# Performance work log

Hardware: AMD Instinct MI355X
Metric: run time of the kernel (lower is better)

Reference implementation:

```python
import jax, jax.numpy as jnp
import numpy as np

N = 524288
L = 16          # num_levels
F = 2           # per_level_dim
T = 1 << 19     # hashmap size per level
BASE, MAXR = 32, 2048
SCALE = np.exp(np.log(MAXR / BASE) / (L - 1))
RES = [int(np.floor(BASE * SCALE ** lv)) + 1 for lv in range(L)]
ACTIVE = 4 * F  # init_active_level * per_level_dim (progressive mask)
D_HID = 64
N_FREQS = 6

_P1 = jnp.uint32(2654435761)
_P2 = jnp.uint32(805459861)
_OFF = jnp.array([[(c >> d) & 1 for d in range(3)] for c in range(8)], dtype=jnp.uint32)  # [8,3]


def setup_inputs() -> dict:
    key = jax.random.key(0)
    ks = jax.random.split(key, 8)
    x = (jax.random.uniform(ks[0], (N, 3)) * 2.0 - 1.0) * 0.999  # inside [-bound, bound]
    v = jax.random.normal(ks[1], (N, 3))
    v = v / jnp.linalg.norm(v, axis=-1, keepdims=True)
    o = jax.random.normal(ks[2], (N, 3))  # unused by forward (kept for signature fidelity)
    table = jax.random.uniform(ks[3], (L, T, F), minval=-1e-4, maxval=1e-4)
    d_in = 3 + 3 * 2 * N_FREQS + L * F  # xyz + fourier + hashgrid = 71
    def lin(k, fi, fo):
        return jax.random.normal(k, (fi, fo)) * np.sqrt(2.0 / fi).astype(np.float32)
    dw1 = lin(ks[4], d_in, D_HID); db1 = jnp.zeros((D_HID,), jnp.float32)
    dw2 = lin(ks[5], D_HID, 1 + D_HID); db2 = jnp.zeros((1 + D_HID,), jnp.float32)
    rw1 = lin(ks[6], D_HID + 9, D_HID); rb1 = jnp.zeros((D_HID,), jnp.float32)
    rw2 = lin(ks[7], D_HID, 3); rb2 = jnp.zeros((3,), jnp.float32)
    return dict(x=x, v=v, o=o, table=table, dw1=dw1, db1=db1, dw2=dw2, db2=db2,
                rw1=rw1, rb1=rb1, rw2=rw2, rb2=rb2)


def hashgrid(x01, table):
    """Multi-res hash encoding with Smoothstep interpolation. x01 in [0,1]^3."""
    feats = []
    for lv in range(L):
        pos = x01 * RES[lv]
        p0 = jnp.floor(pos)
        t = pos - p0
        w = t * t * (3.0 - 2.0 * t)                       # smoothstep weights [N,3]
        corner = p0.astype(jnp.uint32)[:, None, :] + _OFF[None]  # [N,8,3]
        h = (corner[..., 0] ^ (corner[..., 1] * _P1) ^ (corner[..., 2] * _P2)) & jnp.uint32(T - 1)
        cw = jnp.prod(jnp.where(_OFF[None] == 1, w[:, None, :], 1.0 - w[:, None, :]), axis=-1)  # [N,8]
        feats.append(jnp.sum(table[lv][h.astype(jnp.int32)] * cw[..., None], axis=1))  # [N,F]
    return jnp.concatenate(feats, axis=-1)  # [N, L*F]


def fourier(x):
    freqs = 2.0 ** jnp.arange(N_FREQS, dtype=x.dtype)  # log-sampled 2^0..2^5
    ang = x[..., None] * freqs                         # [N,3,6]
    return jnp.concatenate([jnp.sin(ang), jnp.cos(ang)], axis=-1).reshape(x.shape[0], -1)


def sh3(d):
    """Spherical harmonics, degree 3 (levels=3) -> 9 features."""
    xx, yy, zz = d[..., 0], d[..., 1], d[..., 2]
    return jnp.stack([
        0.28209479177387814 * jnp.ones_like(xx),
        -0.4886025119029199 * yy, 0.4886025119029199 * zz, -0.4886025119029199 * xx,
        1.0925484305920792 * xx * yy, -1.0925484305920792 * yy * zz,
        0.9461746957575601 * zz * zz - 0.31539156525252005,
        -1.0925484305920792 * xx * zz,
        0.5462742152960396 * (xx * xx - yy * yy)], axis=-1)


def reference(x, v, o, table, dw1, db1, dw2, db2, rw1, rb1, rw2, rb2):
    x01 = (x + 1.0) * 0.5  # bound = 1.0
    grid = hashgrid(x01, table)
    mask = (jnp.arange(L * F) < ACTIVE).astype(grid.dtype)  # progressive level mask
    x_enc = jnp.concatenate([x, fourier(x), grid * mask], axis=-1)  # [N,71]
    h = jax.nn.relu(x_enc @ dw1 + db1)
    dout = h @ dw2 + db2                 # [N, 1 + d_hidden]
    sigma = jnp.exp(dout[..., :1])       # trunc_exp forward == exp
    feat = jax.nn.relu(dout[..., 1:])
    rgb_in = jnp.concatenate([feat, sh3(v)], axis=-1)  # [N, 73]
    hr = jax.nn.relu(rgb_in @ rw1 + rb1)
    rgb = jax.nn.sigmoid(hr @ rw2 + rb2)
    return sigma, rgb
```

## Files before the change

### kernel.cpp

```cpp
#include <hip/hip_runtime.h>

#define NPTS   524288
#define TBLM   ((1u << 19) - 1u)
#define THR    512
#define CHUNK  128
#define CHUNKS 4
#define GRID   (NPTS / (CHUNK * CHUNKS))

typedef _Float16 half8  __attribute__((ext_vector_type(8)));
typedef _Float16 half4v __attribute__((ext_vector_type(4)));
typedef float    f32x4  __attribute__((ext_vector_type(4)));


__global__ __launch_bounds__(256)
void prep(const float* __restrict__ dw1, const float* __restrict__ db1,
          const float* __restrict__ dw2, const float* __restrict__ db2,
          const float* __restrict__ rw1, const float* __restrict__ rb1,
          const float* __restrict__ rw2, const float* __restrict__ rb2,
          void* __restrict__ ws)
{
    const int t = blockIdx.x * 256 + threadIdx.x;
    if (t < 16384) {
        float w = 0.0f;
        if (t < 4096) {
            const int u = t, mkc = u >> 9, m = mkc >> 1, kc = mkc & 1;
            const int lane = (u >> 3) & 63, j = u & 7;
            const int row = 16 * m + (lane & 15);
            const int kp  = kc * 32 + (lane >> 4) * 8 + j;
            if (kp < 39)      w = dw1[kp * 64 + row];
            else if (kp == 39) w = 0.0f;
            else if (kp < 48) w = dw1[(kp - 1) * 64 + row];
        } else if (t < 9216) {
            const int u = t - 4096, mkc = u >> 9, m = mkc >> 1, kc = mkc & 1;
            const int lane = (u >> 3) & 63, j = u & 7;
            const int row = 16 * m + (lane & 15);
            const int k   = kc * 32 + (lane >> 4) * 8 + j;
            if (row < 65) w = dw2[k * 65 + row];
        } else if (t < 15360) {
            const int u = t - 9216, mkc = u >> 9, m = mkc / 3, kc = mkc - 3 * m;
            const int lane = (u >> 3) & 63, j = u & 7;
            const int row = 16 * m + (lane & 15);
            const int kp  = kc * 32 + (lane >> 4) * 8 + j;
            if (kp >= 1 && kp <= 73) w = rw1[(kp - 1) * 64 + row];
        } else {
            const int u = t - 15360, kc = u >> 9;
            const int lane = (u >> 3) & 63, j = u & 7;
            const int row = lane & 15;
            const int k   = kc * 32 + (lane >> 4) * 8 + j;
            if (row < 3) w = rw2[k * 3 + row];
        }
        ((_Float16*)ws)[t] = (_Float16)w;
    } else if (t < 16384 + 224) {
        const int u = t - 16384;
        float b = 0.0f;
        if (u < 64)        b = db1[u];
        else if (u < 144)  { const int r = u - 64;  if (r < 65) b = db2[r]; }
        else if (u < 208)  b = rb1[u - 144];
        else               { const int r = u - 208; if (r < 3)  b = rb2[r]; }
        ((float*)((char*)ws + 32768))[u] = b;
    }
}

__device__ __forceinline__ float sstep(float t) { return t * t * (3.0f - 2.0f * t); }

__global__ __launch_bounds__(THR, 4)
void nerf_fwd(const float* __restrict__ x,
              const float* __restrict__ v,
              const float* __restrict__ table,
              const float* __restrict__ ws,
              float* __restrict__ out)
{
    __shared__ __align__(16) unsigned char smem[78720];
    _Float16* wt    = (_Float16*)smem;
    float*    sbias = (float*)(smem + 32768);
    _Float16* aB    = (_Float16*)(smem + 33664);
    _Float16* bB    = (_Float16*)(smem + 60288);

    const int tid  = threadIdx.x;
    const int lane = tid & 63;
    const int wv   = tid >> 6;
    const int lr   = lane & 15;
    const int lg   = lane >> 4;

    {
        const uint4* src = (const uint4*)ws;
        uint4* dst = (uint4*)smem;
        #pragma unroll
        for (int i = 0; i < 5; ++i) {
            const int idx = tid + i * THR;
            if (idx < 2104) dst[idx] = src[idx];
        }
    }
    __syncthreads();

    const int gi0 = blockIdx.x * (CHUNK * CHUNKS);

    for (int c = 0; c < CHUNKS; ++c) {
        const int cbase = gi0 + c * CHUNK;

        {
            const int p    = (wv << 4) + (lane >> 2);
            const int gi   = cbase + p;
            const int role = lane & 3;
            _Float16* row = aB + p * 104;
            if (role == 3) {
                const float v0 = v[3 * gi + 0], v1 = v[3 * gi + 1], v2 = v[3 * gi + 2];
                float sh[9];
                sh[0] = 0.28209479177387814f;
                sh[1] = -0.4886025119029199f * v1;
                sh[2] =  0.4886025119029199f * v2;
                sh[3] = -0.4886025119029199f * v0;
                sh[4] =  1.0925484305920792f * v0 * v1;
                sh[5] = -1.0925484305920792f * v1 * v2;
                sh[6] =  0.9461746957575601f * v2 * v2 - 0.31539156525252005f;
                sh[7] = -1.0925484305920792f * v0 * v2;
                sh[8] =  0.5462742152960396f * (v0 * v0 - v1 * v1);
                half8 s0, s1, z;
                s0[0] = (_Float16)0.f;
                #pragma unroll
                for (int i = 0; i < 7; ++i) s0[i + 1] = (_Float16)sh[i];
                s1[0] = (_Float16)sh[7]; s1[1] = (_Float16)sh[8];
                #pragma unroll
                for (int i = 2; i < 8; ++i) s1[i] = (_Float16)0.f;
                #pragma unroll
                for (int i = 0; i < 8; ++i) z[i] = (_Float16)0.f;
                *(half8*)(row + 48) = z;
                *(half8*)(row + 56) = z;
                *(half8*)(row + 64) = s0;
                *(half8*)(row + 72) = s1;
                *(half8*)(row + 80) = z;
                *(half8*)(row + 88) = z;
            } else {
                const float x0 = x[3 * gi + 0], x1 = x[3 * gi + 1], x2 = x[3 * gi + 2];
                if (role == 0) {
                    float e[40];
                    e[0] = x0; e[1] = x1; e[2] = x2;
                    const float a[3] = {x0, x1, x2};
                    #pragma unroll
                    for (int d = 0; d < 3; ++d)
                        #pragma unroll
                        for (int f = 0; f < 6; ++f) {
                            const float ang = a[d] * (float)(1 << f);
                            e[3 + d * 12 + f]     = __sinf(ang);
                            e[3 + d * 12 + 6 + f] = __cosf(ang);
                        }
                    e[39] = 0.0f;
                    #pragma unroll
                    for (int chk = 0; chk < 5; ++chk) {
                        half8 h;
                        #pragma unroll
                        for (int i = 0; i < 8; ++i) h[i] = (_Float16)e[chk * 8 + i];
                        *(half8*)(row + chk * 8) = h;
                    }
                } else {
                    const float u0 = (x0 + 1.0f) * 0.5f, u1 = (x1 + 1.0f) * 0.5f, u2 = (x2 + 1.0f) * 0.5f;
                    const float rfA = (role == 1) ? 33.0f : 56.0f;
                    const float rfB = (role == 1) ? 43.0f : 74.0f;
                    const unsigned lvA = (role == 1) ? 0u : 2u;
                    float g[4];
                    #pragma unroll
                    for (int s = 0; s < 2; ++s) {
                        const float rf = s ? rfB : rfA;
                        const unsigned lv = lvA + (unsigned)s;
                        const float px = u0 * rf, py = u1 * rf, pz = u2 * rf;
                        const float fx = floorf(px), fy = floorf(py), fz = floorf(pz);
                        const float wx = sstep(px - fx), wy = sstep(py - fy), wz = sstep(pz - fz);
                        const unsigned cx = (unsigned)fx, cy = (unsigned)fy, cz = (unsigned)fz;
                        float g0 = 0.f, g1 = 0.f;
                        #pragma unroll
                        for (int cc = 0; cc < 8; ++cc) {
                            const unsigned hx = cx + (cc & 1);
                            const unsigned hy = cy + ((cc >> 1) & 1);
                            const unsigned hz = cz + ((cc >> 2) & 1);
                            const unsigned hh = (hx ^ (hy * 2654435761u) ^ (hz * 805459861u)) & TBLM;
                            const float2 tv = *reinterpret_cast<const float2*>(
                                table + (lv * (TBLM + 1u) + hh) * 2u);
                            const float cw = ((cc & 1) ? wx : 1.0f - wx) *
                                             ((cc & 2) ? wy : 1.0f - wy) *
                                             ((cc & 4) ? wz : 1.0f - wz);
                            g0 = fmaf(cw, tv.x, g0);
                            g1 = fmaf(cw, tv.y, g1);
                        }
                        g[2 * s]     = g0;
                        g[2 * s + 1] = g1;
                    }
                    half4v h4;
                    #pragma unroll
                    for (int i = 0; i < 4; ++i) h4[i] = (_Float16)g[i];
                    *(half4v*)(row + 40 + (role - 1) * 4) = h4;
                }
            }
        }

        const int pt = (wv << 4) + lr;

        {
            const half8 B0 = *(const half8*)(aB + pt * 104 + 0 * 32 + lg * 8);
            const half8 B1 = *(const half8*)(aB + pt * 104 + 1 * 32 + lg * 8);
            #pragma unroll
            for (int m = 0; m < 4; ++m) {
                const half8 A0 = *(const half8*)(wt + (m * 2 + 0) * 512 + lane * 8);
                const half8 A1 = *(const half8*)(wt + (m * 2 + 1) * 512 + lane * 8);
                f32x4 cr = *(const f32x4*)(sbias + 0 + m * 16 + 4 * lg);
                cr = __builtin_amdgcn_mfma_f32_16x16x32_f16(A0, B0, cr, 0, 0, 0);
                cr = __builtin_amdgcn_mfma_f32_16x16x32_f16(A1, B1, cr, 0, 0, 0);
                half4v o4;
                #pragma unroll
                for (int r = 0; r < 4; ++r) o4[r] = (_Float16)fmaxf(cr[r], 0.f);
                *(half4v*)(bB + pt * 72 + 16 * m + 4 * lg) = o4;
            }
        }

        {
            const half8 B0 = *(const half8*)(bB + pt * 72 + 0 * 32 + lg * 8);
            const half8 B1 = *(const half8*)(bB + pt * 72 + 1 * 32 + lg * 8);
            #pragma unroll
            for (int m = 0; m < 4; ++m) {
                const half8 A0 = *(const half8*)(wt + 4096 + (m * 2 + 0) * 512 + lane * 8);
                const half8 A1 = *(const half8*)(wt + 4096 + (m * 2 + 1) * 512 + lane * 8);
                f32x4 cr = *(const f32x4*)(sbias + 64 + m * 16 + 4 * lg);
                cr = __builtin_amdgcn_mfma_f32_16x16x32_f16(A0, B0, cr, 0, 0, 0);
                cr = __builtin_amdgcn_mfma_f32_16x16x32_f16(A1, B1, cr, 0, 0, 0);
                half4v o4;
                #pragma unroll
                for (int r = 0; r < 4; ++r) o4[r] = (_Float16)fmaxf(cr[r], 0.f);
                *(half4v*)(aB + pt * 104 + 16 * m + 4 * lg) = o4;
                if (m == 0 && lg == 0)
                    out[cbase + pt] = __expf(cr[0]);
            }
            {
                const half8 A0 = *(const half8*)(wt + 4096 + (4 * 2 + 0) * 512 + lane * 8);
                const half8 A1 = *(const half8*)(wt + 4096 + (4 * 2 + 1) * 512 + lane * 8);
                f32x4 cr = *(const f32x4*)(sbias + 64 + 4 * 16 + 4 * lg);
                cr = __builtin_amdgcn_mfma_f32_16x16x32_f16(A0, B0, cr, 0, 0, 0);
                cr = __builtin_amdgcn_mfma_f32_16x16x32_f16(A1, B1, cr, 0, 0, 0);
                if (lg == 0) aB[pt * 104 + 64] = (_Float16)fmaxf(cr[0], 0.f);
            }
        }

        {
            const half8 B0 = *(const half8*)(aB + pt * 104 + 0 * 32 + lg * 8);
            const half8 B1 = *(const half8*)(aB + pt * 104 + 1 * 32 + lg * 8);
            const half8 B2 = *(const half8*)(aB + pt * 104 + 2 * 32 + lg * 8);
            #pragma unroll
            for (int m = 0; m < 4; ++m) {
                const half8 A0 = *(const half8*)(wt + 9216 + (m * 3 + 0) * 512 + lane * 8);
                const half8 A1 = *(const half8*)(wt + 9216 + (m * 3 + 1) * 512 + lane * 8);
                const half8 A2 = *(const half8*)(wt + 9216 + (m * 3 + 2) * 512 + lane * 8);
                f32x4 cr = *(const f32x4*)(sbias + 144 + m * 16 + 4 * lg);
                cr = __builtin_amdgcn_mfma_f32_16x16x32_f16(A0, B0, cr, 0, 0, 0);
                cr = __builtin_amdgcn_mfma_f32_16x16x32_f16(A1, B1, cr, 0, 0, 0);
                cr = __builtin_amdgcn_mfma_f32_16x16x32_f16(A2, B2, cr, 0, 0, 0);
                half4v o4;
                #pragma unroll
                for (int r = 0; r < 4; ++r) o4[r] = (_Float16)fmaxf(cr[r], 0.f);
                *(half4v*)(bB + pt * 72 + 16 * m + 4 * lg) = o4;
            }
        }

        {
            const half8 A0 = *(const half8*)(wt + 15360 + 0 * 512 + lane * 8);
            const half8 A1 = *(const half8*)(wt + 15360 + 1 * 512 + lane * 8);
            const half8 B0 = *(const half8*)(bB + pt * 72 + 0 * 32 + lg * 8);
            const half8 B1 = *(const half8*)(bB + pt * 72 + 1 * 32 + lg * 8);
            f32x4 cr = *(const f32x4*)(sbias + 208 + 4 * lg);
            cr = __builtin_amdgcn_mfma_f32_16x16x32_f16(A0, B0, cr, 0, 0, 0);
            cr = __builtin_amdgcn_mfma_f32_16x16x32_f16(A1, B1, cr, 0, 0, 0);
            if (lg == 0) {
                const int gpt = cbase + pt;
                #pragma unroll
                for (int r = 0; r < 3; ++r)
                    out[NPTS + 3 * gpt + r] = 1.0f / (1.0f + __expf(-cr[r]));
            }
        }
    }
}

extern "C" void kernel_launch(void* const* d_in, const int* in_sizes, int n_in,
                              void* d_out, int out_size, void* d_ws, size_t ws_size,
                              hipStream_t stream) {
    const float* x     = (const float*)d_in[0];
    const float* v     = (const float*)d_in[1];
    const float* table = (const float*)d_in[3];
    const float* dw1   = (const float*)d_in[4];
    const float* db1   = (const float*)d_in[5];
    const float* dw2   = (const float*)d_in[6];
    const float* db2   = (const float*)d_in[7];
    const float* rw1   = (const float*)d_in[8];
    const float* rb1   = (const float*)d_in[9];
    const float* rw2   = (const float*)d_in[10];
    const float* rb2   = (const float*)d_in[11];
    float* out = (float*)d_out;

    hipLaunchKernelGGL(prep, dim3(65), dim3(256), 0, stream,
                       dw1, db1, dw2, db2, rw1, rb1, rw2, rb2, d_ws);
    hipLaunchKernelGGL(nerf_fwd, dim3(GRID), dim3(THR), 0, stream,
                       x, v, table, (const float*)d_ws, out);
}
```

Baseline: 191.5 us.

## Prefetch next chunk's hash-table gathers during MLP and rebalance encoding roles

Splits the encoding into a gather-issue phase and a finish phase, and issues the next chunk's x/v loads and hash-table gathers before running the current chunk's MFMA layers, so gather latency overlaps compute. The first chunk's gathers are issued before the weight copy to shared memory. It also gives each of the four lanes per point one hash level (8 gathers each) instead of two lanes doing two levels, and spreads the Fourier, SH and zero-fill work across roles. The cost is more live registers for the prefetched state, which may pressure occupancy at 4 blocks of 512 threads.

```diff
diff --git a/kernel.cpp b/kernel.cpp
--- a/kernel.cpp
+++ b/kernel.cpp
@@ -9,6 +9,7 @@
 
 typedef _Float16 half8  __attribute__((ext_vector_type(8)));
 typedef _Float16 half4v __attribute__((ext_vector_type(4)));
+typedef _Float16 half2v __attribute__((ext_vector_type(2)));
 typedef float    f32x4  __attribute__((ext_vector_type(4)));
 
 
@@ -63,6 +64,114 @@
 
 __device__ __forceinline__ float sstep(float t) { return t * t * (3.0f - 2.0f * t); }
 
+struct GS {
+    float  x0, x1, x2, v0, v1, v2;
+    float  ax, ay, az;
+    float2 t0, t1, t2, t3, t4, t5, t6, t7;
+};
+
+__device__ __forceinline__ void gather_issue(int gi, int role,
+    const float* __restrict__ x, const float* __restrict__ v,
+    const float* __restrict__ table, GS& s)
+{
+    s.x0 = x[3 * gi + 0]; s.x1 = x[3 * gi + 1]; s.x2 = x[3 * gi + 2];
+    if (role == 1) { s.v0 = v[3 * gi + 0]; s.v1 = v[3 * gi + 1]; s.v2 = v[3 * gi + 2]; }
+    const float rf = (role == 0) ? 33.f : (role == 1) ? 43.f : (role == 2) ? 56.f : 74.f;
+    const float u0 = (s.x0 + 1.f) * 0.5f, u1 = (s.x1 + 1.f) * 0.5f, u2 = (s.x2 + 1.f) * 0.5f;
+    const float px = u0 * rf, py = u1 * rf, pz = u2 * rf;
+    const float fx = floorf(px), fy = floorf(py), fz = floorf(pz);
+    s.ax = sstep(px - fx); s.ay = sstep(py - fy); s.az = sstep(pz - fz);
+    const unsigned cx = (unsigned)fx, cy = (unsigned)fy, cz = (unsigned)fz;
+    const float* tb = table + (unsigned)role * (TBLM + 1u) * 2u;
+    const unsigned hy0 = cy * 2654435761u, hy1 = (cy + 1u) * 2654435761u;
+    const unsigned hz0 = cz * 805459861u,  hz1 = (cz + 1u) * 805459861u;
+#define LDC(dst, HX, HY, HZ) { const unsigned hh = ((HX) ^ (HY) ^ (HZ)) & TBLM; \
+                               dst = *reinterpret_cast<const float2*>(tb + hh * 2u); }
+    LDC(s.t0, cx,      hy0, hz0);
+    LDC(s.t1, cx + 1u, hy0, hz0);
+    LDC(s.t2, cx,      hy1, hz0);
+    LDC(s.t3, cx + 1u, hy1, hz0);
+    LDC(s.t4, cx,      hy0, hz1);
+    LDC(s.t5, cx + 1u, hy0, hz1);
+    LDC(s.t6, cx,      hy1, hz1);
+    LDC(s.t7, cx + 1u, hy1, hz1);
+#undef LDC
+}
+
+__device__ __forceinline__ void encode_finish(const GS& s, int role, _Float16* row)
+{
+    const float ax = s.ax, ay = s.ay, az = s.az;
+    const float bx = 1.f - ax, by = 1.f - ay, bz = 1.f - az;
+    const float p00 = bx * by, p10 = ax * by, p01 = bx * ay, p11 = ax * ay;
+    const float w0 = p00 * bz, w1 = p10 * bz, w2 = p01 * bz, w3 = p11 * bz;
+    const float w4 = p00 * az, w5 = p10 * az, w6 = p01 * az, w7 = p11 * az;
+    float g0 = w0 * s.t0.x, g1 = w0 * s.t0.y;
+    g0 = fmaf(w1, s.t1.x, g0); g1 = fmaf(w1, s.t1.y, g1);
+    g0 = fmaf(w2, s.t2.x, g0); g1 = fmaf(w2, s.t2.y, g1);
+    g0 = fmaf(w3, s.t3.x, g0); g1 = fmaf(w3, s.t3.y, g1);
+    g0 = fmaf(w4, s.t4.x, g0); g1 = fmaf(w4, s.t4.y, g1);
+    g0 = fmaf(w5, s.t5.x, g0); g1 = fmaf(w5, s.t5.y, g1);
+    g0 = fmaf(w6, s.t6.x, g0); g1 = fmaf(w6, s.t6.y, g1);
+    g0 = fmaf(w7, s.t7.x, g0); g1 = fmaf(w7, s.t7.y, g1);
+    half2v gh; gh[0] = (_Float16)g0; gh[1] = (_Float16)g1;
+    *(half2v*)(row + 40 + 2 * role) = gh;
+
+    if (role == 0) {
+        float e[40];
+        e[0] = s.x0; e[1] = s.x1; e[2] = s.x2;
+        const float a[3] = {s.x0, s.x1, s.x2};
+        #pragma unroll
+        for (int d = 0; d < 3; ++d)
+            #pragma unroll
+            for (int f = 0; f < 6; ++f) {
+                const float ang = a[d] * (float)(1 << f);
+                e[3 + d * 12 + f]     = __sinf(ang);
+                e[3 + d * 12 + 6 + f] = __cosf(ang);
+            }
+        e[39] = 0.0f;
+        #pragma unroll
+        for (int chk = 0; chk < 5; ++chk) {
+            half8 h;
+            #pragma unroll
+            for (int i = 0; i < 8; ++i) h[i] = (_Float16)e[chk * 8 + i];
+            *(half8*)(row + chk * 8) = h;
+        }
+    } else if (role == 1) {
+        const float v0 = s.v0, v1 = s.v1, v2 = s.v2;
+        float sh[9];
+        sh[0] = 0.28209479177387814f;
+        sh[1] = -0.4886025119029199f * v1;
+        sh[2] =  0.4886025119029199f * v2;
+        sh[3] = -0.4886025119029199f * v0;
+        sh[4] =  1.0925484305920792f * v0 * v1;
+        sh[5] = -1.0925484305920792f * v1 * v2;
+        sh[6] =  0.9461746957575601f * v2 * v2 - 0.31539156525252005f;
+        sh[7] = -1.0925484305920792f * v0 * v2;
+        sh[8] =  0.5462742152960396f * (v0 * v0 - v1 * v1);
+        half8 s0, s1;
+        s0[0] = (_Float16)0.f;
+        #pragma unroll
+        for (int i = 0; i < 7; ++i) s0[i + 1] = (_Float16)sh[i];
+        s1[0] = (_Float16)sh[7]; s1[1] = (_Float16)sh[8];
+        #pragma unroll
+        for (int i = 2; i < 8; ++i) s1[i] = (_Float16)0.f;
+        *(half8*)(row + 64) = s0;
+        *(half8*)(row + 72) = s1;
+    } else if (role == 2) {
+        half8 z;
+        #pragma unroll
+        for (int i = 0; i < 8; ++i) z[i] = (_Float16)0.f;
+        *(half8*)(row + 48) = z;
+        *(half8*)(row + 56) = z;
+    } else {
+        half8 z;
+        #pragma unroll
+        for (int i = 0; i < 8; ++i) z[i] = (_Float16)0.f;
+        *(half8*)(row + 80) = z;
+        *(half8*)(row + 88) = z;
+    }
+}
+
 __global__ __launch_bounds__(THR, 4)
 void nerf_fwd(const float* __restrict__ x,
               const float* __restrict__ v,
@@ -81,6 +190,12 @@
     const int wv   = tid >> 6;
     const int lr   = lane & 15;
     const int lg   = lane >> 4;
+    const int role = lane & 3;
+    const int ep   = (wv << 4) + (lane >> 2);
+    const int gi0  = blockIdx.x * (CHUNK * CHUNKS);
+
+    GS cur, nxt;
+    gather_issue(gi0 + ep, role, x, v, table, cur);
 
     {
         const uint4* src = (const uint4*)ws;
@@ -93,106 +208,16 @@
     }
     __syncthreads();
 
-    const int gi0 = blockIdx.x * (CHUNK * CHUNKS);
-
+    const int pt = (wv << 4) + lr;
+
+    #pragma unroll
     for (int c = 0; c < CHUNKS; ++c) {
         const int cbase = gi0 + c * CHUNK;
 
-        {
-            const int p    = (wv << 4) + (lane >> 2);
-            const int gi   = cbase + p;
-            const int role = lane & 3;
-            _Float16* row = aB + p * 104;
-            if (role == 3) {
-                const float v0 = v[3 * gi + 0], v1 = v[3 * gi + 1], v2 = v[3 * gi + 2];
-                float sh[9];
-                sh[0] = 0.28209479177387814f;
-                sh[1] = -0.4886025119029199f * v1;
-                sh[2] =  0.4886025119029199f * v2;
-                sh[3] = -0.4886025119029199f * v0;
-                sh[4] =  1.0925484305920792f * v0 * v1;
-                sh[5] = -1.0925484305920792f * v1 * v2;
-                sh[6] =  0.9461746957575601f * v2 * v2 - 0.31539156525252005f;
-                sh[7] = -1.0925484305920792f * v0 * v2;
-                sh[8] =  0.5462742152960396f * (v0 * v0 - v1 * v1);
-                half8 s0, s1, z;
-                s0[0] = (_Float16)0.f;
-                #pragma unroll
-                for (int i = 0; i < 7; ++i) s0[i + 1] = (_Float16)sh[i];
-                s1[0] = (_Float16)sh[7]; s1[1] = (_Float16)sh[8];
-                #pragma unroll
-                for (int i = 2; i < 8; ++i) s1[i] = (_Float16)0.f;
-                #pragma unroll
-                for (int i = 0; i < 8; ++i) z[i] = (_Float16)0.f;
-                *(half8*)(row + 48) = z;
-                *(half8*)(row + 56) = z;
-                *(half8*)(row + 64) = s0;
-                *(half8*)(row + 72) = s1;
-                *(half8*)(row + 80) = z;
-                *(half8*)(row + 88) = z;
-            } else {
-                const float x0 = x[3 * gi + 0], x1 = x[3 * gi + 1], x2 = x[3 * gi + 2];
-                if (role == 0) {
-                    float e[40];
-                    e[0] = x0; e[1] = x1; e[2] = x2;
-                    const float a[3] = {x0, x1, x2};
-                    #pragma unroll
-                    for (int d = 0; d < 3; ++d)
-                        #pragma unroll
-                        for (int f = 0; f < 6; ++f) {
-                            const float ang = a[d] * (float)(1 << f);
-                            e[3 + d * 12 + f]     = __sinf(ang);
-                            e[3 + d * 12 + 6 + f] = __cosf(ang);
-                        }
-                    e[39] = 0.0f;
-                    #pragma unroll
-                    for (int chk = 0; chk < 5; ++chk) {
-                        half8 h;
-                        #pragma unroll
-                        for (int i = 0; i < 8; ++i) h[i] = (_Float16)e[chk * 8 + i];
-                        *(half8*)(row + chk * 8) = h;
-                    }
-                } else {
-                    const float u0 = (x0 + 1.0f) * 0.5f, u1 = (x1 + 1.0f) * 0.5f, u2 = (x2 + 1.0f) * 0.5f;
-                    const float rfA = (role == 1) ? 33.0f : 56.0f;
-                    const float rfB = (role == 1) ? 43.0f : 74.0f;
-                    const unsigned lvA = (role == 1) ? 0u : 2u;
-                    float g[4];
-                    #pragma unroll
-                    for (int s = 0; s < 2; ++s) {
-                        const float rf = s ? rfB : rfA;
-                        const unsigned lv = lvA + (unsigned)s;
-                        const float px = u0 * rf, py = u1 * rf, pz = u2 * rf;
-                        const float fx = floorf(px), fy = floorf(py), fz = floorf(pz);
-                        const float wx = sstep(px - fx), wy = sstep(py - fy), wz = sstep(pz - fz);
-                        const unsigned cx = (unsigned)fx, cy = (unsigned)fy, cz = (unsigned)fz;
-                        float g0 = 0.f, g1 = 0.f;
-                        #pragma unroll
-                        for (int cc = 0; cc < 8; ++cc) {
-                            const unsigned hx = cx + (cc & 1);
-                            const unsigned hy = cy + ((cc >> 1) & 1);
-                            const unsigned hz = cz + ((cc >> 2) & 1);
-                            const unsigned hh = (hx ^ (hy * 2654435761u) ^ (hz * 805459861u)) & TBLM;
-                            const float2 tv = *reinterpret_cast<const float2*>(
-                                table + (lv * (TBLM + 1u) + hh) * 2u);
-                            const float cw = ((cc & 1) ? wx : 1.0f - wx) *
-                                             ((cc & 2) ? wy : 1.0f - wy) *
-                                             ((cc & 4) ? wz : 1.0f - wz);
-                            g0 = fmaf(cw, tv.x, g0);
-                            g1 = fmaf(cw, tv.y, g1);
-                        }
-                        g[2 * s]     = g0;
-                        g[2 * s + 1] = g1;
-                    }
-                    half4v h4;
-                    #pragma unroll
-                    for (int i = 0; i < 4; ++i) h4[i] = (_Float16)g[i];
-                    *(half4v*)(row + 40 + (role - 1) * 4) = h4;
-                }
-            }
-        }
-
-        const int pt = (wv << 4) + lr;
+        encode_finish(cur, role, aB + ep * 104);
+
+        if (c + 1 < CHUNKS)
+            gather_issue(gi0 + (c + 1) * CHUNK + ep, role, x, v, table, nxt);
 
         {
             const half8 B0 = *(const half8*)(aB + pt * 104 + 0 * 32 + lg * 8);
@@ -273,6 +298,8 @@
                     out[NPTS + 3 * gpt + r] = 1.0f / (1.0f + __expf(-cr[r]));
             }
         }
+
+        if (c + 1 < CHUNKS) cur = nxt;
     }
 }
 
```

Result: no change. 187.8 us (-1.9%).
